# Optimization experiments

Measured on AMD Instinct MI355X. Metric: run time of the kernel, lower is better.

Reference implementation:

```python
import jax, jax.numpy as jnp
import numpy as np

B, T, C = 2, 2048, 2048
NUM_HEADS, NUM_KV_HEADS, HEAD_DIM = 16, 4, 128
ROPE_THETA = 10000.0
SOFTCAP = 50.0


def sine_table(features, length, min_timescale=1.0, max_timescale=10000.0):
    fraction = jnp.arange(0, features, 2, dtype=jnp.float32) / features
    timescale = min_timescale * (max_timescale / min_timescale) ** fraction
    sinusoid = jnp.arange(length, dtype=jnp.float32)[:, None] / timescale[None, :]
    sinusoid = jnp.concatenate([sinusoid, sinusoid], axis=-1)
    return jnp.sin(sinusoid), jnp.cos(sinusoid)


def rotate_half(x):
    x1, x2 = jnp.split(x, 2, axis=-1)
    return jnp.concatenate([-x2, x1], axis=-1)


def setup_inputs() -> dict:
    key = jax.random.key(0)
    k1, k2, k3, k4, k5 = jax.random.split(key, 5)
    x = jax.random.normal(k1, (B, T, C), dtype=jnp.float32)
    mask = jnp.tril(jnp.ones((T, T), dtype=bool))[None, None]  # causal [1,1,T,T]
    mask = jnp.broadcast_to(mask, (B, 1, T, T))
    std = 0.02
    q_kernel = std * jax.random.normal(k2, (C, NUM_HEADS * HEAD_DIM), dtype=jnp.float32)
    k_kernel = std * jax.random.normal(k3, (C, NUM_KV_HEADS * HEAD_DIM), dtype=jnp.float32)
    v_kernel = std * jax.random.normal(k4, (C, NUM_KV_HEADS * HEAD_DIM), dtype=jnp.float32)
    out_kernel = std * jax.random.normal(k5, (NUM_HEADS * HEAD_DIM, C), dtype=jnp.float32)
    return {"x": x, "mask": mask, "q_kernel": q_kernel, "k_kernel": k_kernel,
            "v_kernel": v_kernel, "out_kernel": out_kernel}


def reference(x, mask, q_kernel, k_kernel, v_kernel, out_kernel):
    _, t, c = x.shape
    r = NUM_HEADS // NUM_KV_HEADS  # GQA group size
    qp = q_kernel.reshape(c, r, NUM_KV_HEADS, HEAD_DIM)
    kp = k_kernel.reshape(c, NUM_KV_HEADS, HEAD_DIM)
    vp = v_kernel.reshape(c, NUM_KV_HEADS, HEAD_DIM)
    op = out_kernel.reshape(r, NUM_KV_HEADS, HEAD_DIM, c)
    q = jnp.einsum('bsm,mrhk->brhsk', x, qp)   # [B,r,h,T,hd]
    k = jnp.einsum('bdm,mhk->bhdk', x, kp)     # [B,h,T,hd]
    v = jnp.einsum('bdm,mhv->bhdv', x, vp)     # [B,h,T,hd]
    sin, cos = sine_table(HEAD_DIM, t, max_timescale=ROPE_THETA)  # [T,hd]
    q = q * cos + rotate_half(q) * sin  # broadcast over leading dims (time at -2)
    k = k * cos + rotate_half(k) * sin
    scale = jax.lax.rsqrt(jnp.array(HEAD_DIM, dtype=x.dtype))
    qk = jnp.einsum('brhsk,bhdk->brhsd', q, k) * scale  # [B,r,h,T,T]
    qk = jnp.tanh(qk / SOFTCAP) * SOFTCAP  # logit softcap
    m = jnp.expand_dims(mask, axis=1)  # [B,1,1,T,T]
    qk = jax.nn.softmax(qk.astype(jnp.float32), where=m).astype(x.dtype)
    qkv = jnp.einsum('brhsd,bhdv->brhsv', qk, v)
    out = jnp.einsum('brhsv,rhvm->bsm', qkv, op)
    return out
```

## Files before the change

### kernel.cpp

```cpp
#include <hip/hip_runtime.h>
#include <hip/hip_bf16.h>

typedef __hip_bfloat16 bf16;
typedef __attribute__((ext_vector_type(8))) short bf16x8;
typedef __attribute__((ext_vector_type(4))) short bf16x4;
typedef __attribute__((ext_vector_type(4))) float f32x4;

#define BATCH 2
#define SEQ 2048
#define CDIM 2048
#define NH 16
#define NKV 4
#define HD 128
#define NQKV 3072

__device__ __forceinline__ float tof(float x)  { return x; }
__device__ __forceinline__ float tof(bf16 x)   { return __bfloat162float(x); }
__device__ __forceinline__ void  stf(float* p, float v) { *p = v; }
__device__ __forceinline__ void  stf(bf16* p,  float v) { *p = __float2bfloat16(v); }

__device__ __forceinline__ void gl_lds16(const bf16* g, bf16* l) {
    typedef const __attribute__((address_space(1))) unsigned int* gp_t;
    typedef __attribute__((address_space(3))) unsigned int* lp_t;
    __builtin_amdgcn_global_load_lds((gp_t)g, (lp_t)l, 16, 0, 0);
}

__device__ __forceinline__ f32x4 mfma16x16x16_bf16(bf16x4 a, bf16x4 b, f32x4 c) {
#if __has_builtin(__builtin_amdgcn_mfma_f32_16x16x16bf16_1k)
    return __builtin_amdgcn_mfma_f32_16x16x16bf16_1k(a, b, c, 0, 0, 0);
#else
    asm volatile("v_mfma_f32_16x16x16_bf16 %0, %1, %2, %0"
                 : "+v"(c) : "v"(a), "v"(b));
    return c;
#endif
}

__device__ __forceinline__ float fast_exp2(float x) {
#if __has_builtin(__builtin_amdgcn_exp2f)
    return __builtin_amdgcn_exp2f(x);
#else
    return exp2f(x);
#endif
}

__global__ __launch_bounds__(256) void f2b_kernel(const float* __restrict__ in,
                                                  bf16* __restrict__ out, int n4)
{
    int i = blockIdx.x * 256 + threadIdx.x;
    if (i >= n4) return;
    float4 v = *(const float4*)&in[(size_t)i * 4];
    bf16 o[4] = {__float2bfloat16(v.x), __float2bfloat16(v.y),
                 __float2bfloat16(v.z), __float2bfloat16(v.w)};
    *(ushort4*)&out[(size_t)i * 4] = *(ushort4*)o;
}

__global__ __launch_bounds__(256) void transpose_f2b_kernel(
    const float* __restrict__ in, bf16* __restrict__ out, int R, int Cn)
{
    __shared__ float tile[64][65];
    const int r0 = blockIdx.y * 64, c0 = blockIdx.x * 64;
    for (int f = threadIdx.x; f < 4096; f += 256) {
        int r = f >> 6, c = f & 63;
        tile[r][c] = in[(size_t)(r0 + r) * Cn + c0 + c];
    }
    __syncthreads();
    for (int f = threadIdx.x; f < 4096; f += 256) {
        int r = f >> 6, c = f & 63;
        out[(size_t)(c0 + r) * R + r0 + c] = __float2bfloat16(tile[c][r]);
    }
}

__global__ __launch_bounds__(256) void vtrans_kernel(
    const bf16* __restrict__ in, bf16* __restrict__ out)
{
    __shared__ bf16 tile[64][65];
    const int b = blockIdx.z;
    const int t0 = blockIdx.y * 64, c0 = blockIdx.x * 64;
    for (int f = threadIdx.x; f < 4096; f += 256) {
        int r = f >> 6, c = f & 63;
        tile[r][c] = in[(size_t)(b * SEQ + t0 + r) * (NKV * HD) + c0 + c];
    }
    __syncthreads();
    for (int f = threadIdx.x; f < 4096; f += 256) {
        int r = f >> 6, c = f & 63;
        out[(size_t)(b * NKV * HD + c0 + r) * SEQ + t0 + c] = tile[c][r];
    }
}

__global__ __launch_bounds__(256) void gemm_qkv_kernel(
    const bf16* __restrict__ A, const bf16* __restrict__ Bt,
    bf16* __restrict__ Qr, bf16* __restrict__ Kr, bf16* __restrict__ Vr,
    int M, int K)
{
    __shared__ __align__(16) bf16 As[128 * 32];
    __shared__ __align__(16) bf16 Bs[128 * 32];

    const int tid = threadIdx.x;
    const int lane = tid & 63;
    const int wave = tid >> 6;
    const int m0 = blockIdx.y * 128;
    const int n0 = blockIdx.x * 128;
    const int wm = (wave >> 1) * 64;
    const int wn = (wave & 1) * 64;
    const int quad = lane >> 4;
    const int l16 = lane & 15;

    const int srow = tid >> 2;
    const int scol = (tid & 3) * 8;
    const bf16* Ag0 = A  + (size_t)(m0 + srow) * K + scol;
    const bf16* Ag1 = A  + (size_t)(m0 + srow + 64) * K + scol;
    const bf16* Bg0 = Bt + (size_t)(n0 + srow) * K + scol;
    const bf16* Bg1 = Bt + (size_t)(n0 + srow + 64) * K + scol;

    f32x4 acc[4][4];
#pragma unroll
    for (int mi = 0; mi < 4; ++mi)
#pragma unroll
        for (int ni = 0; ni < 4; ++ni)
            acc[mi][ni] = (f32x4){0.f, 0.f, 0.f, 0.f};

    for (int kt = 0; kt < K; kt += 32) {
        __syncthreads();
        gl_lds16(Ag0 + kt, &As[tid * 8]);
        gl_lds16(Ag1 + kt, &As[2048 + tid * 8]);
        gl_lds16(Bg0 + kt, &Bs[tid * 8]);
        gl_lds16(Bg1 + kt, &Bs[2048 + tid * 8]);
        __syncthreads();

        bf16x8 a[4], b[4];
#pragma unroll
        for (int mi = 0; mi < 4; ++mi)
            a[mi] = *(const bf16x8*)&As[(wm + mi * 16 + l16) * 32 + quad * 8];
#pragma unroll
        for (int ni = 0; ni < 4; ++ni)
            b[ni] = *(const bf16x8*)&Bs[(wn + ni * 16 + l16) * 32 + quad * 8];
#pragma unroll
        for (int mi = 0; mi < 4; ++mi)
#pragma unroll
            for (int ni = 0; ni < 4; ++ni)
                acc[mi][ni] = __builtin_amdgcn_mfma_f32_16x16x32_bf16(
                    a[mi], b[ni], acc[mi][ni], 0, 0, 0);
    }

    bf16* Cp; int Nst, cbase;
    if (n0 < 2048)      { Cp = Qr; Nst = 2048; cbase = n0; }
    else if (n0 < 2560) { Cp = Kr; Nst = 512;  cbase = n0 - 2048; }
    else                { Cp = Vr; Nst = 512;  cbase = n0 - 2560; }

#pragma unroll
    for (int mi = 0; mi < 4; ++mi)
#pragma unroll
        for (int ni = 0; ni < 4; ++ni) {
            int col = cbase + wn + ni * 16 + l16;
#pragma unroll
            for (int r = 0; r < 4; ++r) {
                int row = m0 + wm + mi * 16 + quad * 4 + r;
                Cp[(size_t)row * Nst + col] = __float2bfloat16(acc[mi][ni][r]);
            }
        }
}

template <typename TC>
__global__ __launch_bounds__(256) void gemm_mfma_bt(
    const bf16* __restrict__ A, const bf16* __restrict__ Bt, TC* __restrict__ C,
    int M, int N, int K)
{
    __shared__ __align__(16) bf16 As[128 * 32];
    __shared__ __align__(16) bf16 Bs[128 * 32];

    const int tid = threadIdx.x;
    const int lane = tid & 63;
    const int wave = tid >> 6;
    const int m0 = blockIdx.y * 128;
    const int n0 = blockIdx.x * 128;
    const int wm = (wave >> 1) * 64;
    const int wn = (wave & 1) * 64;
    const int quad = lane >> 4;
    const int l16 = lane & 15;

    const int srow = tid >> 2;
    const int scol = (tid & 3) * 8;
    const bf16* Ag0 = A  + (size_t)(m0 + srow) * K + scol;
    const bf16* Ag1 = A  + (size_t)(m0 + srow + 64) * K + scol;
    const bf16* Bg0 = Bt + (size_t)(n0 + srow) * K + scol;
    const bf16* Bg1 = Bt + (size_t)(n0 + srow + 64) * K + scol;

    f32x4 acc[4][4];
#pragma unroll
    for (int mi = 0; mi < 4; ++mi)
#pragma unroll
        for (int ni = 0; ni < 4; ++ni)
            acc[mi][ni] = (f32x4){0.f, 0.f, 0.f, 0.f};

    for (int kt = 0; kt < K; kt += 32) {
        __syncthreads();
        gl_lds16(Ag0 + kt, &As[tid * 8]);
        gl_lds16(Ag1 + kt, &As[2048 + tid * 8]);
        gl_lds16(Bg0 + kt, &Bs[tid * 8]);
        gl_lds16(Bg1 + kt, &Bs[2048 + tid * 8]);
        __syncthreads();

        bf16x8 a[4], b[4];
#pragma unroll
        for (int mi = 0; mi < 4; ++mi)
            a[mi] = *(const bf16x8*)&As[(wm + mi * 16 + l16) * 32 + quad * 8];
#pragma unroll
        for (int ni = 0; ni < 4; ++ni)
            b[ni] = *(const bf16x8*)&Bs[(wn + ni * 16 + l16) * 32 + quad * 8];
#pragma unroll
        for (int mi = 0; mi < 4; ++mi)
#pragma unroll
            for (int ni = 0; ni < 4; ++ni)
                acc[mi][ni] = __builtin_amdgcn_mfma_f32_16x16x32_bf16(
                    a[mi], b[ni], acc[mi][ni], 0, 0, 0);
    }

#pragma unroll
    for (int mi = 0; mi < 4; ++mi)
#pragma unroll
        for (int ni = 0; ni < 4; ++ni) {
            int col = n0 + wn + ni * 16 + l16;
#pragma unroll
            for (int r = 0; r < 4; ++r) {
                int row = m0 + wm + mi * 16 + quad * 4 + r;
                stf(&C[(size_t)row * N + col], acc[mi][ni][r]);
            }
        }
}

__global__ __launch_bounds__(256) void rope_kernel(bf16* __restrict__ data,
                                                   int ncols, int total_pairs)
{
    int idx = blockIdx.x * 256 + threadIdx.x;
    if (idx >= total_pairs) return;
    int half = ncols >> 1;
    int row = idx / half;
    int p = idx - row * half;
    int head = p >> 6;
    int i = p & 63;
    int t = row & (SEQ - 1);
    float inv_ts = expf(-(float)i * 0.14391156831212787f);
    float angle = (float)t * inv_ts;
    float s, c;
    sincosf(angle, &s, &c);
    size_t base = (size_t)row * ncols + head * 128 + i;
    float x1 = __bfloat162float(data[base]);
    float x2 = __bfloat162float(data[base + 64]);
    data[base]      = __float2bfloat16(x1 * c - x2 * s);
    data[base + 64] = __float2bfloat16(x2 * c + x1 * s);
}

__global__ __launch_bounds__(256, 3) void attn_mfma6_kernel(
    const bf16* __restrict__ Q, const bf16* __restrict__ K,
    const bf16* __restrict__ Vt, bf16* __restrict__ Att)
{
    __shared__ __align__(16) char smem[32768];
    bf16* Ks  = (bf16*)smem;
    bf16* Vts = (bf16*)(smem + 16384);

    const int tid = threadIdx.x;
    const int lane = tid & 63;
    const int w = tid >> 6;
    const int hs = w >> 1;
    const int qw = w & 1;
    const int quad = lane >> 4;
    const int l16 = lane & 15;
    const int bh = blockIdx.y;
    const int b   = bh >> 3;
    const int kvh = (bh >> 1) & 3;
    const int pr  = bh & 1;
    const int hq  = kvh + 4 * (pr * 2 + hs);
    const int qt = (gridDim.x - 1) - blockIdx.x;
    const int q0 = qt * 32 + qw * 16;

    bf16x8 qf[4];
    {
        size_t qrow = (size_t)(b * SEQ + q0 + l16) * (NH * HD) + hq * HD;
#pragma unroll
        for (int kk = 0; kk < 4; ++kk)
            qf[kk] = *(const bf16x8*)&Q[qrow + kk * 32 + quad * 8];
    }

    const bf16* Kb = K  + (size_t)(b * SEQ) * (NKV * HD) + kvh * HD;
    const bf16* Vb = Vt + (size_t)((b * NKV + kvh) * HD) * SEQ;

    f32x4 O[8];
#pragma unroll
    for (int dj = 0; dj < 8; ++dj) O[dj] = (f32x4){0.f, 0.f, 0.f, 0.f};
    float lsum = 0.f;

    const int srowK = tid >> 4;
    const int sgcK  = (tid & 15) ^ srowK;
    const int srowV = tid >> 3;
    const int sgcV  = (tid & 7) ^ (srowV & 7);

    const int ntiles = (qt >> 1) + 1;
    const int qsel = (qt & 1) * 32 + qw * 16 + l16;
    for (int jt = 0; jt < ntiles; ++jt) {
        const int j0 = jt * 64;
        __syncthreads();
#pragma unroll
        for (int c = 0; c < 4; ++c) {
            gl_lds16(Kb + (size_t)(j0 + c * 16 + srowK) * (NKV * HD) + sgcK * 8,
                     Ks + c * 2048 + tid * 8);
            gl_lds16(Vb + (size_t)(c * 32 + srowV) * SEQ + j0 + sgcV * 8,
                     Vts + c * 2048 + tid * 8);
        }
        __syncthreads();

        const bool diag = (jt == (qt >> 1));
#pragma unroll
        for (int half = 0; half < 2; ++half) {
            f32x4 sacc[2];
#pragma unroll
            for (int mt = 0; mt < 2; ++mt) {
                sacc[mt] = (f32x4){0.f, 0.f, 0.f, 0.f};
                const int krow = (half * 32 + mt * 16 + l16) * 128;
#pragma unroll
                for (int kk = 0; kk < 4; ++kk) {
                    bf16x8 kf = *(const bf16x8*)&Ks[krow + (((kk * 4 + quad) ^ l16) * 8)];
                    sacc[mt] = __builtin_amdgcn_mfma_f32_16x16x32_bf16(
                        kf, qf[kk], sacc[mt], 0, 0, 0);
                }
            }

            bf16x4 pf[2];
#pragma unroll
            for (int mt = 0; mt < 2; ++mt) {
                bf16 pb[4];
#pragma unroll
                for (int r = 0; r < 4; ++r) {
                    float u = sacc[mt][r];
                    float t2 = u * u;
                    float num = fmaf(t2, 9.96274e-4f, 8607.814f);
                    float den = fmaf(t2, 0.0703125f, 67500.f);
                    float s2 = u * num * __builtin_amdgcn_rcpf(den);
                    float p = fast_exp2(s2);
                    if (diag) {
                        int kl = half * 32 + mt * 16 + quad * 4 + r;
                        p = (kl <= qsel) ? p : 0.f;
                    }
                    lsum += p;
                    pb[r] = __float2bfloat16(p);
                }
                pf[mt] = *(bf16x4*)pb;
            }

#pragma unroll
            for (int dj = 0; dj < 8; ++dj) {
                const int vrow = (dj * 16 + l16) * 64;
                const int dl7 = l16 & 7;
#pragma unroll
                for (int mt = 0; mt < 2; ++mt) {
                    int c16 = half * 4 + mt * 2 + (quad >> 1);
                    bf16x4 vf = *(const bf16x4*)&Vts[vrow + ((c16 ^ dl7) << 3)
                                                     + (quad & 1) * 4];
                    O[dj] = mfma16x16x16_bf16(vf, pf[mt], O[dj]);
                }
            }
        }
    }

    {
        float v = lsum;
        v += __shfl_xor(v, 16);
        v += __shfl_xor(v, 32);
        float inv = 1.f / v;
        size_t obase = (size_t)(b * SEQ + q0 + l16) * (NH * HD) + hq * HD;
#pragma unroll
        for (int dj = 0; dj < 8; ++dj) {
            bf16 ob[4];
#pragma unroll
            for (int r = 0; r < 4; ++r)
                ob[r] = __float2bfloat16(O[dj][r] * inv);
            *(ushort4*)&Att[obase + dj * 16 + quad * 4] = *(ushort4*)ob;
        }
    }
}

extern "C" void kernel_launch(void* const* d_in, const int* in_sizes, int n_in,
                              void* d_out, int out_size, void* d_ws, size_t ws_size,
                              hipStream_t stream) {
    const float* x        = (const float*)d_in[0];
    const float* q_kernel = (const float*)d_in[2];
    const float* k_kernel = (const float*)d_in[3];
    const float* v_kernel = (const float*)d_in[4];
    const float* o_kernel = (const float*)d_in[5];
    float* out = (float*)d_out;

    const int M = BATCH * SEQ;
    char* ws = (char*)d_ws;
    bf16* xb   = (bf16*)ws;
    bf16* Att  = xb;
    bf16* wT   = (bf16*)(ws + 16777216);
    bf16* wTq  = wT;
    bf16* wTk  = wT + (size_t)2048 * 2048;
    bf16* wTv  = wT + (size_t)2560 * 2048;
    bf16* woT  = wT;
    bf16* Vt_g = (bf16*)(ws + 25165824);
    bf16* Qr   = (bf16*)(ws + 29360128);
    bf16* Kr   = (bf16*)(ws + 46137344);
    bf16* Vr   = (bf16*)(ws + 50331648);

    f2b_kernel<<<(M * CDIM / 4 + 255) / 256, 256, 0, stream>>>(x, xb, M * CDIM / 4);
    transpose_f2b_kernel<<<dim3((NH * HD) / 64, CDIM / 64), 256, 0, stream>>>(
        q_kernel, wTq, CDIM, NH * HD);
    transpose_f2b_kernel<<<dim3((NKV * HD) / 64, CDIM / 64), 256, 0, stream>>>(
        k_kernel, wTk, CDIM, NKV * HD);
    transpose_f2b_kernel<<<dim3((NKV * HD) / 64, CDIM / 64), 256, 0, stream>>>(
        v_kernel, wTv, CDIM, NKV * HD);

    gemm_qkv_kernel<<<dim3(NQKV / 128, M / 128), 256, 0, stream>>>(
        xb, wT, Qr, Kr, Vr, M, CDIM);

    transpose_f2b_kernel<<<dim3(CDIM / 64, CDIM / 64), 256, 0, stream>>>(
        o_kernel, woT, CDIM, CDIM);

    {
        int pairs_q = M * (NH * HD / 2);
        rope_kernel<<<pairs_q / 256, 256, 0, stream>>>(Qr, NH * HD, pairs_q);
        int pairs_k = M * (NKV * HD / 2);
        rope_kernel<<<pairs_k / 256, 256, 0, stream>>>(Kr, NKV * HD, pairs_k);
    }

    vtrans_kernel<<<dim3((NKV * HD) / 64, SEQ / 64, BATCH), 256, 0, stream>>>(Vr, Vt_g);

    attn_mfma6_kernel<<<dim3(SEQ / 32, BATCH * NKV * 2), 256, 0, stream>>>(
        Qr, Kr, Vt_g, Att);

    gemm_mfma_bt<float><<<dim3(CDIM / 128, M / 128), 256, 0, stream>>>(
        Att, woT, out, M, CDIM, CDIM);
}
```

Baseline: 395.8 us.

## Pair low/high causal query tiles per block and double-buffer K/V loads

Each attention block now processes two query tiles, a low one and its mirror high one, so every block does the same amount of causal work and K/V tiles loaded into LDS are shared by both. K/V tile loads are double-buffered in 64KB of LDS, so the next tile is prefetched while the current one is computed, leaving one barrier per iteration. The grid is halved and occupancy drops to two blocks per CU. Register pressure roughly doubles because there are two sets of output accumulators and Q fragments.

```diff
diff --git a/kernel.cpp b/kernel.cpp
--- a/kernel.cpp
+++ b/kernel.cpp
@@ -41,6 +41,14 @@
 #else
     return exp2f(x);
 #endif
+}
+
+__device__ __forceinline__ float softcap_exp(float u) {
+    float t2 = u * u;
+    float num = fmaf(t2, 9.96274e-4f, 8607.814f);
+    float den = fmaf(t2, 0.0703125f, 67500.f);
+    float s2 = u * num * __builtin_amdgcn_rcpf(den);
+    return fast_exp2(s2);
 }
 
 __global__ __launch_bounds__(256) void f2b_kernel(const float* __restrict__ in,
@@ -250,13 +258,83 @@
     data[base + 64] = __float2bfloat16(x2 * c + x1 * s);
 }
 
-__global__ __launch_bounds__(256, 3) void attn_mfma6_kernel(
+template <bool WA>
+__device__ __forceinline__ void attn_tile_compute(
+    const bf16* __restrict__ Ksr, const bf16* __restrict__ Vtsr,
+    const bf16x8 (&qfA)[4], const bf16x8 (&qfB)[4],
+    f32x4 (&OA)[8], f32x4 (&OB)[8], float& lsumA, float& lsumB,
+    int quad, int l16, bool diagA, bool diagB, int qselA, int qselB)
+{
+#pragma unroll
+    for (int half = 0; half < 2; ++half) {
+        f32x4 sA[2], sB[2];
+        bf16x4 pfA[2], pfB[2];
+#pragma unroll
+        for (int mt = 0; mt < 2; ++mt) {
+            sB[mt] = (f32x4){0.f, 0.f, 0.f, 0.f};
+            if constexpr (WA) sA[mt] = (f32x4){0.f, 0.f, 0.f, 0.f};
+            const int krow = (half * 32 + mt * 16 + l16) * 128;
+#pragma unroll
+            for (int kk = 0; kk < 4; ++kk) {
+                bf16x8 kf = *(const bf16x8*)&Ksr[krow + (((kk * 4 + quad) ^ l16) * 8)];
+                sB[mt] = __builtin_amdgcn_mfma_f32_16x16x32_bf16(
+                    kf, qfB[kk], sB[mt], 0, 0, 0);
+                if constexpr (WA)
+                    sA[mt] = __builtin_amdgcn_mfma_f32_16x16x32_bf16(
+                        kf, qfA[kk], sA[mt], 0, 0, 0);
+            }
+        }
+#pragma unroll
+        for (int mt = 0; mt < 2; ++mt) {
+            bf16 pb[4];
+#pragma unroll
+            for (int r = 0; r < 4; ++r) {
+                float p = softcap_exp(sB[mt][r]);
+                if (diagB) {
+                    int kl = half * 32 + mt * 16 + quad * 4 + r;
+                    p = (kl <= qselB) ? p : 0.f;
+                }
+                lsumB += p;
+                pb[r] = __float2bfloat16(p);
+            }
+            pfB[mt] = *(bf16x4*)pb;
+            if constexpr (WA) {
+                bf16 pa[4];
+#pragma unroll
+                for (int r = 0; r < 4; ++r) {
+                    float p = softcap_exp(sA[mt][r]);
+                    if (diagA) {
+                        int kl = half * 32 + mt * 16 + quad * 4 + r;
+                        p = (kl <= qselA) ? p : 0.f;
+                    }
+                    lsumA += p;
+                    pa[r] = __float2bfloat16(p);
+                }
+                pfA[mt] = *(bf16x4*)pa;
+            }
+        }
+#pragma unroll
+        for (int dj = 0; dj < 8; ++dj) {
+            const int vrow = (dj * 16 + l16) * 64;
+            const int dl7 = l16 & 7;
+#pragma unroll
+            for (int mt = 0; mt < 2; ++mt) {
+                int c16 = half * 4 + mt * 2 + (quad >> 1);
+                bf16x4 vf = *(const bf16x4*)&Vtsr[vrow + ((c16 ^ dl7) << 3)
+                                                  + (quad & 1) * 4];
+                OB[dj] = mfma16x16x16_bf16(vf, pfB[mt], OB[dj]);
+                if constexpr (WA)
+                    OA[dj] = mfma16x16x16_bf16(vf, pfA[mt], OA[dj]);
+            }
+        }
+    }
+}
+
+__global__ __launch_bounds__(256, 2) void attn_mfma7_kernel(
     const bf16* __restrict__ Q, const bf16* __restrict__ K,
     const bf16* __restrict__ Vt, bf16* __restrict__ Att)
 {
-    __shared__ __align__(16) char smem[32768];
-    bf16* Ks  = (bf16*)smem;
-    bf16* Vts = (bf16*)(smem + 16384);
+    __shared__ __align__(16) char smem[65536];
 
     const int tid = threadIdx.x;
     const int lane = tid & 63;
@@ -270,109 +348,111 @@
     const int kvh = (bh >> 1) & 3;
     const int pr  = bh & 1;
     const int hq  = kvh + 4 * (pr * 2 + hs);
-    const int qt = (gridDim.x - 1) - blockIdx.x;
-    const int q0 = qt * 32 + qw * 16;
-
-    bf16x8 qf[4];
+    const int qlo = blockIdx.x;
+    const int qhi = 63 - qlo;
+    const int ntlo = (qlo >> 1) + 1;
+    const int nthi = (qhi >> 1) + 1;
+    const int q0A = qlo * 32 + qw * 16;
+    const int q0B = qhi * 32 + qw * 16;
+
+    bf16x8 qfA[4], qfB[4];
     {
-        size_t qrow = (size_t)(b * SEQ + q0 + l16) * (NH * HD) + hq * HD;
-#pragma unroll
-        for (int kk = 0; kk < 4; ++kk)
-            qf[kk] = *(const bf16x8*)&Q[qrow + kk * 32 + quad * 8];
+        size_t ra = (size_t)(b * SEQ + q0A + l16) * (NH * HD) + hq * HD;
+        size_t rb = (size_t)(b * SEQ + q0B + l16) * (NH * HD) + hq * HD;
+#pragma unroll
+        for (int kk = 0; kk < 4; ++kk) {
+            qfA[kk] = *(const bf16x8*)&Q[ra + kk * 32 + quad * 8];
+            qfB[kk] = *(const bf16x8*)&Q[rb + kk * 32 + quad * 8];
+        }
     }
 
     const bf16* Kb = K  + (size_t)(b * SEQ) * (NKV * HD) + kvh * HD;
     const bf16* Vb = Vt + (size_t)((b * NKV + kvh) * HD) * SEQ;
 
-    f32x4 O[8];
-#pragma unroll
-    for (int dj = 0; dj < 8; ++dj) O[dj] = (f32x4){0.f, 0.f, 0.f, 0.f};
-    float lsum = 0.f;
+    f32x4 OA[8], OB[8];
+#pragma unroll
+    for (int dj = 0; dj < 8; ++dj) {
+        OA[dj] = (f32x4){0.f, 0.f, 0.f, 0.f};
+        OB[dj] = (f32x4){0.f, 0.f, 0.f, 0.f};
+    }
+    float lsumA = 0.f, lsumB = 0.f;
 
     const int srowK = tid >> 4;
     const int sgcK  = (tid & 15) ^ srowK;
     const int srowV = tid >> 3;
     const int sgcV  = (tid & 7) ^ (srowV & 7);
 
-    const int ntiles = (qt >> 1) + 1;
-    const int qsel = (qt & 1) * 32 + qw * 16 + l16;
-    for (int jt = 0; jt < ntiles; ++jt) {
-        const int j0 = jt * 64;
+    const int qselA = (qlo & 1) * 32 + qw * 16 + l16;
+    const int qselB = (qhi & 1) * 32 + qw * 16 + l16;
+
+    {
+        bf16* KsW  = (bf16*)smem;
+        bf16* VtsW = (bf16*)(smem + 32768);
+#pragma unroll
+        for (int c = 0; c < 4; ++c) {
+            gl_lds16(Kb + (size_t)(c * 16 + srowK) * (NKV * HD) + sgcK * 8,
+                     KsW + c * 2048 + tid * 8);
+            gl_lds16(Vb + (size_t)(c * 32 + srowV) * SEQ + sgcV * 8,
+                     VtsW + c * 2048 + tid * 8);
+        }
+    }
+    __syncthreads();
+
+    int cur = 0;
+    for (int jt = 0; jt < nthi; ++jt) {
+        if (jt + 1 < nthi) {
+            const int j0 = (jt + 1) * 64;
+            bf16* KsW  = (bf16*)(smem + (cur ^ 1) * 16384);
+            bf16* VtsW = (bf16*)(smem + 32768 + (cur ^ 1) * 16384);
+#pragma unroll
+            for (int c = 0; c < 4; ++c) {
+                gl_lds16(Kb + (size_t)(j0 + c * 16 + srowK) * (NKV * HD) + sgcK * 8,
+                         KsW + c * 2048 + tid * 8);
+                gl_lds16(Vb + (size_t)(c * 32 + srowV) * SEQ + j0 + sgcV * 8,
+                         VtsW + c * 2048 + tid * 8);
+            }
+        }
+        const bf16* Ksr  = (const bf16*)(smem + cur * 16384);
+        const bf16* Vtsr = (const bf16*)(smem + 32768 + cur * 16384);
+        const bool diagA = (jt == ntlo - 1);
+        const bool diagB = (jt == nthi - 1);
+        if (jt < ntlo)
+            attn_tile_compute<true>(Ksr, Vtsr, qfA, qfB, OA, OB, lsumA, lsumB,
+                                    quad, l16, diagA, diagB, qselA, qselB);
+        else
+            attn_tile_compute<false>(Ksr, Vtsr, qfA, qfB, OA, OB, lsumA, lsumB,
+                                     quad, l16, diagA, diagB, qselA, qselB);
         __syncthreads();
-#pragma unroll
-        for (int c = 0; c < 4; ++c) {
-            gl_lds16(Kb + (size_t)(j0 + c * 16 + srowK) * (NKV * HD) + sgcK * 8,
-                     Ks + c * 2048 + tid * 8);
-            gl_lds16(Vb + (size_t)(c * 32 + srowV) * SEQ + j0 + sgcV * 8,
-                     Vts + c * 2048 + tid * 8);
-        }
-        __syncthreads();
-
-        const bool diag = (jt == (qt >> 1));
-#pragma unroll
-        for (int half = 0; half < 2; ++half) {
-            f32x4 sacc[2];
-#pragma unroll
-            for (int mt = 0; mt < 2; ++mt) {
-                sacc[mt] = (f32x4){0.f, 0.f, 0.f, 0.f};
-                const int krow = (half * 32 + mt * 16 + l16) * 128;
-#pragma unroll
-                for (int kk = 0; kk < 4; ++kk) {
-                    bf16x8 kf = *(const bf16x8*)&Ks[krow + (((kk * 4 + quad) ^ l16) * 8)];
-                    sacc[mt] = __builtin_amdgcn_mfma_f32_16x16x32_bf16(
-                        kf, qf[kk], sacc[mt], 0, 0, 0);
-                }
-            }
-
-            bf16x4 pf[2];
-#pragma unroll
-            for (int mt = 0; mt < 2; ++mt) {
-                bf16 pb[4];
-#pragma unroll
-                for (int r = 0; r < 4; ++r) {
-                    float u = sacc[mt][r];
-                    float t2 = u * u;
-                    float num = fmaf(t2, 9.96274e-4f, 8607.814f);
-                    float den = fmaf(t2, 0.0703125f, 67500.f);
-                    float s2 = u * num * __builtin_amdgcn_rcpf(den);
-                    float p = fast_exp2(s2);
-                    if (diag) {
-                        int kl = half * 32 + mt * 16 + quad * 4 + r;
-                        p = (kl <= qsel) ? p : 0.f;
-                    }
-                    lsum += p;
-                    pb[r] = __float2bfloat16(p);
-                }
-                pf[mt] = *(bf16x4*)pb;
-            }
-
-#pragma unroll
-            for (int dj = 0; dj < 8; ++dj) {
-                const int vrow = (dj * 16 + l16) * 64;
-                const int dl7 = l16 & 7;
-#pragma unroll
-                for (int mt = 0; mt < 2; ++mt) {
-                    int c16 = half * 4 + mt * 2 + (quad >> 1);
-                    bf16x4 vf = *(const bf16x4*)&Vts[vrow + ((c16 ^ dl7) << 3)
-                                                     + (quad & 1) * 4];
-                    O[dj] = mfma16x16x16_bf16(vf, pf[mt], O[dj]);
-                }
-            }
-        }
+        cur ^= 1;
     }
 
     {
-        float v = lsum;
+        float v = lsumA;
         v += __shfl_xor(v, 16);
         v += __shfl_xor(v, 32);
         float inv = 1.f / v;
-        size_t obase = (size_t)(b * SEQ + q0 + l16) * (NH * HD) + hq * HD;
+        size_t obase = (size_t)(b * SEQ + q0A + l16) * (NH * HD) + hq * HD;
 #pragma unroll
         for (int dj = 0; dj < 8; ++dj) {
             bf16 ob[4];
 #pragma unroll
             for (int r = 0; r < 4; ++r)
-                ob[r] = __float2bfloat16(O[dj][r] * inv);
+                ob[r] = __float2bfloat16(OA[dj][r] * inv);
+            *(ushort4*)&Att[obase + dj * 16 + quad * 4] = *(ushort4*)ob;
+        }
+    }
+    {
+        float v = lsumB;
+        v += __shfl_xor(v, 16);
+        v += __shfl_xor(v, 32);
+        float inv = 1.f / v;
+        size_t obase = (size_t)(b * SEQ + q0B + l16) * (NH * HD) + hq * HD;
+#pragma unroll
+        for (int dj = 0; dj < 8; ++dj) {
+            bf16 ob[4];
+#pragma unroll
+            for (int r = 0; r < 4; ++r)
+                ob[r] = __float2bfloat16(OB[dj][r] * inv);
             *(ushort4*)&Att[obase + dj * 16 + quad * 4] = *(ushort4*)ob;
         }
     }
@@ -425,7 +505,7 @@
 
     vtrans_kernel<<<dim3((NKV * HD) / 64, SEQ / 64, BATCH), 256, 0, stream>>>(Vr, Vt_g);
 
-    attn_mfma6_kernel<<<dim3(SEQ / 32, BATCH * NKV * 2), 256, 0, stream>>>(
+    attn_mfma7_kernel<<<dim3(SEQ / 64, BATCH * NKV * 2), 256, 0, stream>>>(
         Qr, Kr, Vt_g, Att);
 
     gemm_mfma_bt<float><<<dim3(CDIM / 128, M / 128), 256, 0, stream>>>(
```

Result: faster. 383.0 us (-3.2%).
